# Optimization experiments

Hardware: AMD Instinct MI355X
Metric: run time of the kernel (lower is better)

Reference implementation:

```python
import jax, jax.numpy as jnp
import numpy as np

MIN_NORM = 1e-15
BALL_EPS = 1e-3   # project() margin from ball boundary (c = 1)
TANH_CLIP = 15.0


def _norm(x):
    return jnp.sqrt(jnp.sum(x * x, axis=-1, keepdims=True)).clip(MIN_NORM)


def _tanh(x):
    return jnp.tanh(jnp.clip(x, -TANH_CLIP, TANH_CLIP))


def _artanh(x):
    return jnp.arctanh(jnp.clip(x, -1.0 + 1e-7, 1.0 - 1e-7))


def mobius_add(x, y):
    # Poincare ball Mobius addition, curvature c = 1
    x2 = jnp.sum(x * x, axis=-1, keepdims=True)
    y2 = jnp.sum(y * y, axis=-1, keepdims=True)
    xy = jnp.sum(x * y, axis=-1, keepdims=True)
    num = (1.0 + 2.0 * xy + y2) * x + (1.0 - x2) * y
    den = 1.0 + 2.0 * xy + x2 * y2
    return num / den.clip(MIN_NORM)


def project(x):
    norm = _norm(x)
    maxnorm = 1.0 - BALL_EPS
    return jnp.where(norm > maxnorm, x * (maxnorm / norm), x)


def expmap0(u):
    # exp map at the origin
    n = _norm(u)
    return _tanh(n) * u / n


def expmap(u, p):
    # exp map of tangent vector u at base point p
    n = _norm(u)
    p2 = jnp.sum(p * p, axis=-1, keepdims=True)
    lam = 2.0 / (1.0 - p2).clip(MIN_NORM)
    second = _tanh(0.5 * lam * n) * u / n
    return mobius_add(p, second)


def logmap(y, x):
    # log map of point y at base point x
    sub = mobius_add(-x, y)
    n = _norm(sub)
    x2 = jnp.sum(x * x, axis=-1, keepdims=True)
    lam = 2.0 / (1.0 - x2).clip(MIN_NORM)
    return (2.0 / lam) * _artanh(n) * sub / n


def setup_inputs() -> dict:
    key = jax.random.key(0)
    k1, k2, k3, k4 = jax.random.split(key, 4)
    n_entities, n_edges, n_rel, d = 100000, 800000, 32, 64
    # scale embeddings down so points stay well inside the unit ball
    ego_embed = 0.1 * jax.random.normal(k1, (n_entities, d), dtype=jnp.float32)
    relation_embed = 0.1 * jax.random.normal(k2, (n_rel, d), dtype=jnp.float32)
    edge_index = jax.random.randint(k3, (2, n_edges), 0, n_entities, dtype=jnp.int64)
    edge_type = jax.random.randint(k4, (n_edges,), 0, n_rel, dtype=jnp.int64)
    return {"ego_embed": ego_embed, "edge_index": edge_index,
            "edge_type": edge_type, "relation_embed": relation_embed}


def reference(ego_embed, edge_index, edge_type, relation_embed):
    head, tail = edge_index[0], edge_index[1]
    n_entities = ego_embed.shape[0]
    head_emb = ego_embed[head]          # [E, d] gather
    tail_emb = ego_embed[tail]          # [E, d] gather
    relation_emb = relation_embed[edge_type]  # [E, d] gather
    hyper_head = expmap0(head_emb)
    hyper_tail = expmap(tail_emb, hyper_head)
    hyper_rel = expmap(relation_emb, hyper_head)
    res = project(mobius_add(hyper_tail, hyper_rel))
    res = logmap(res, hyper_head)
    # scatter_mean over head index
    sums = jax.ops.segment_sum(res, head, num_segments=n_entities)
    counts = jax.ops.segment_sum(jnp.ones((head.shape[0],), dtype=res.dtype),
                                 head, num_segments=n_entities)
    entity_agg = sums / jnp.maximum(counts, 1.0)[:, None]
    return entity_agg
```

## Files before the change

kernel.cpp:

```cpp
#include <hip/hip_runtime.h>
#include <math.h>

#define D 64
#define MAXNORM 0.999f
#define MAXNORM2 (0.999f * 0.999f)
#define MIN_NORM 1e-15f
#define TANH_CLIP 15.0f
#define CHUNK 1024

struct f4 { float x, y, z, w; };

__device__ __forceinline__ float frcp(float x) { return __builtin_amdgcn_rcpf(x); }
__device__ __forceinline__ float frsq(float x) { return __builtin_amdgcn_rsqf(x); }

__device__ __forceinline__ float dot8p(const f4& a0, const f4& a1,
                                       const f4& b0, const f4& b1) {
    return a0.x * b0.x + a0.y * b0.y + a0.z * b0.z + a0.w * b0.w +
           a1.x * b1.x + a1.y * b1.y + a1.z * b1.z + a1.w * b1.w;
}

__device__ __forceinline__ float rsum8(float v) {
    v += __shfl_xor(v, 1);
    v += __shfl_xor(v, 2);
    v += __shfl_xor(v, 4);
    return v;
}


__global__ void setup_kernel(const float* __restrict__ ego,
                             const float* __restrict__ rel,
                             const int* __restrict__ eidx,
                             int* __restrict__ cnt,
                             int* __restrict__ rank,
                             float* __restrict__ norms,
                             float* __restrict__ relnorm,
                             int N, int E, int hist_blocks) {
    int b = blockIdx.x;
    if (b < hist_blocks) {
        int e = b * 256 + threadIdx.x;
        if (e < E) rank[e] = atomicAdd(&cnt[eidx[e]], 1);
        return;
    }
    int wid = (b - hist_blocks) * 4 + (threadIdx.x >> 6);
    int lane = threadIdx.x & 63;
    const float* src;
    float* dst;
    if (wid < N)            { src = ego + (size_t)wid * D;       dst = norms + wid; }
    else if (wid < N + 32)  { src = rel + (size_t)(wid - N) * D; dst = relnorm + (wid - N); }
    else return;
    float v = src[lane];
    float s = v * v;
    s += __shfl_xor(s, 1);  s += __shfl_xor(s, 2);  s += __shfl_xor(s, 4);
    s += __shfl_xor(s, 8);  s += __shfl_xor(s, 16); s += __shfl_xor(s, 32);
    if (lane == 0) *dst = sqrtf(s);
}


__global__ void scan_kernel(const int* __restrict__ cnt,
                            int* __restrict__ off, int N) {
    __shared__ int sdata[256];
    __shared__ int sprefix;
    int tid = threadIdx.x;
    int base0 = blockIdx.x * CHUNK;

    int psum = 0;
    const int4* cnt4 = (const int4*)cnt;
    for (int i = tid; i < (base0 >> 2); i += 256) {
        int4 v = cnt4[i];
        psum += v.x + v.y + v.z + v.w;
    }
    sdata[tid] = psum;
    __syncthreads();
    for (int o = 128; o > 0; o >>= 1) {
        if (tid < o) sdata[tid] += sdata[tid + o];
        __syncthreads();
    }
    if (tid == 0) sprefix = sdata[0];
    __syncthreads();
    int prefix = sprefix;
    __syncthreads();

    int base = base0 + tid * 4;
    int v0 = (base + 0 < N) ? cnt[base + 0] : 0;
    int v1 = (base + 1 < N) ? cnt[base + 1] : 0;
    int v2 = (base + 2 < N) ? cnt[base + 2] : 0;
    int v3 = (base + 3 < N) ? cnt[base + 3] : 0;
    sdata[tid] = v0 + v1 + v2 + v3;
    __syncthreads();
    for (int o = 1; o < 256; o <<= 1) {
        int add = (tid >= o) ? sdata[tid - o] : 0;
        __syncthreads();
        sdata[tid] += add;
        __syncthreads();
    }
    int run = prefix + ((tid > 0) ? sdata[tid - 1] : 0);
    if (base + 0 < N) { off[base + 0] = run; run += v0; }
    if (base + 1 < N) { off[base + 1] = run; run += v1; }
    if (base + 2 < N) { off[base + 2] = run; run += v2; }
    if (base + 3 < N) { off[base + 3] = run; run += v3; }
}

__global__ void scatter_kernel(const int* __restrict__ eidx,
                               const int* __restrict__ etype,
                               const int* __restrict__ rank,
                               const int* __restrict__ off,
                               int* __restrict__ sorted, int E) {
    int e = blockIdx.x * blockDim.x + threadIdx.x;
    if (e < E) {
        int pos = off[eidx[e]] + rank[e];
        sorted[pos] = eidx[E + e] | (etype[e] << 17);
    }
}


__global__ void __launch_bounds__(256) agg_kernel(
        const float* __restrict__ ego,
        const float* __restrict__ rel,
        const int* __restrict__ off,
        const int* __restrict__ cnt,
        const int* __restrict__ sorted,
        const float* __restrict__ norms,
        const float* __restrict__ relnorm,
        float* __restrict__ out,
        int N) {
    int wid = (blockIdx.x * blockDim.x + threadIdx.x) >> 6;
    if (wid >= N) return;
    int lane = threadIdx.x & 63;
    int slot = lane >> 3;
    int sub  = lane & 7;

    int h = wid;
    const float* hrow = ego + (size_t)h * D + sub * 8;
    f4 h0 = *(const f4*)(hrow);
    f4 h1 = *(const f4*)(hrow + 4);

    float nh  = fmaxf(norms[h], MIN_NORM);
    float xh  = fminf(nh, TANH_CLIP);
    float eh  = __expf(-2.0f * xh);
    float fp  = (1.0f - eh) * frcp((1.0f + eh) * nh);
    float p2  = fp * fp * nh * nh;
    float tol = fmaxf(1.0f - p2, MIN_NORM);
    float hl  = frcp(tol);

    int o = off[h];
    int c = cnt[h];
    f4 a0 = {0.f, 0.f, 0.f, 0.f}, a1 = {0.f, 0.f, 0.f, 0.f};
    float accP = 0.f;

    for (int i = slot; i < c; i += 8) {
        int pk   = sorted[o + i];
        int tail = pk & 0x1FFFF;
        int type = pk >> 17;

        const float* trow = ego + (size_t)tail * D + sub * 8;
        f4 t0 = *(const f4*)(trow);
        f4 t1 = *(const f4*)(trow + 4);
        const float* rrow = rel + (size_t)type * D + sub * 8;
        f4 r0 = *(const f4*)(rrow);
        f4 r1 = *(const f4*)(rrow + 4);
        float nt = norms[tail];
        float nr = relnorm[type];

        float d_ht = rsum8(dot8p(h0, h1, t0, t1));
        float d_hr = rsum8(dot8p(h0, h1, r0, r1));
        float d_tr = rsum8(dot8p(t0, t1, r0, r1));

        float t2 = nt * nt, r2 = nr * nr;
        float pt = fp * d_ht;
        float pr = fp * d_hr;

        float ntc = fmaxf(nt, MIN_NORM);
        float xt  = fminf(hl * ntc, TANH_CLIP);
        float et  = __expf(-2.0f * xt);
        float ft  = (1.0f - et) * frcp((1.0f + et) * ntc);
        float yt2 = ft * ft * t2;
        float pyt = ft * pt;
        float invt = frcp(fmaxf(1.0f + 2.0f * pyt + p2 * yt2, MIN_NORM));
        float At = (1.0f + 2.0f * pyt + yt2) * invt;
        float Bt = tol * invt * ft;
        float x2 = (p2 + 2.0f * pyt + yt2) * invt;

        float nrc = fmaxf(nr, MIN_NORM);
        float xr  = fminf(hl * nrc, TANH_CLIP);
        float er  = __expf(-2.0f * xr);
        float fr  = (1.0f - er) * frcp((1.0f + er) * nrc);
        float yr2 = fr * fr * r2;
        float pyr = fr * pr;
        float invr = frcp(fmaxf(1.0f + 2.0f * pyr + p2 * yr2, MIN_NORM));
        float Ar = (1.0f + 2.0f * pyr + yr2) * invr;
        float Br = tol * invr * fr;
        float y2 = (p2 + 2.0f * pyr + yr2) * invr;

        float xy = At * Ar * p2 + At * Br * pr + Ar * Bt * pt + Bt * Br * d_tr;
        float am = 1.0f + 2.0f * xy + y2;
        float bm = 1.0f - x2;
        float invm = frcp(fmaxf(1.0f + 2.0f * xy + x2 * y2, MIN_NORM));
        float al = (am * At + bm * Ar) * invm;
        float be = am * Bt * invm;
        float ga = bm * Br * invm;
        float m2 = (x2 + 2.0f * xy + y2) * invm;
        m2 = fmaxf(m2, 1e-30f);

        float scp = (m2 > MAXNORM2) ? MAXNORM * frsq(m2) : 1.0f;
        al *= scp; be *= scp; ga *= scp;
        m2 *= scp * scp;

        float pm   = al * p2 + be * pt + ga * pr;
        float invs = frcp(fmaxf(1.0f - 2.0f * pm + p2 * m2, MIN_NORM));
        float sp   = -(1.0f - 2.0f * pm + m2) * invs;
        float smm  = tol * invs;
        float u = sp + smm * al;
        float v = smm * be;
        float w = smm * ga;
        float s2 = (p2 - 2.0f * pm + m2) * invs;
        s2 = fmaxf(s2, 1e-30f);

        float irs = frsq(s2);
        float ns  = fminf(s2 * irs, 1.0f - 1e-7f);
        float art = 0.5f * __logf((1.0f + ns) * frcp(1.0f - ns));
        float sc  = tol * art * irs;

        float ct = sc * v, cr = sc * w;
        accP += sc * u;
        a0.x += ct * t0.x + cr * r0.x;  a0.y += ct * t0.y + cr * r0.y;
        a0.z += ct * t0.z + cr * r0.z;  a0.w += ct * t0.w + cr * r0.w;
        a1.x += ct * t1.x + cr * r1.x;  a1.y += ct * t1.y + cr * r1.y;
        a1.z += ct * t1.z + cr * r1.z;  a1.w += ct * t1.w + cr * r1.w;
    }

    #define RED(x) x += __shfl_xor(x, 8); x += __shfl_xor(x, 16); x += __shfl_xor(x, 32);
    RED(accP)
    RED(a0.x) RED(a0.y) RED(a0.z) RED(a0.w)
    RED(a1.x) RED(a1.y) RED(a1.z) RED(a1.w)
    #undef RED

    if (slot == 0) {
        float invc = frcp(fmaxf((float)c, 1.0f));
        float hp = accP * fp * invc;
        f4 o0, o1;
        o0.x = hp * h0.x + a0.x * invc;  o0.y = hp * h0.y + a0.y * invc;
        o0.z = hp * h0.z + a0.z * invc;  o0.w = hp * h0.w + a0.w * invc;
        o1.x = hp * h1.x + a1.x * invc;  o1.y = hp * h1.y + a1.y * invc;
        o1.z = hp * h1.z + a1.z * invc;  o1.w = hp * h1.w + a1.w * invc;
        float* orow = out + (size_t)h * D + sub * 8;
        *(f4*)(orow)     = o0;
        *(f4*)(orow + 4) = o1;
    }
}

extern "C" void kernel_launch(void* const* d_in, const int* in_sizes, int n_in,
                              void* d_out, int out_size, void* d_ws, size_t ws_size,
                              hipStream_t stream) {
    const float* ego  = (const float*)d_in[0];
    const int*   eidx = (const int*)d_in[1];
    const int*   etyp = (const int*)d_in[2];
    const float* rel  = (const float*)d_in[3];
    float* out = (float*)d_out;

    int E = in_sizes[1] / 2;
    int N = in_sizes[0] / D;
    int NB = (N + CHUNK - 1) / CHUNK;

    int* cnt      = (int*)d_ws;
    int* off      = cnt + N;
    int* rank     = off + N;
    int* sorted   = rank + E;
    float* norms   = (float*)(sorted + E);
    float* relnorm = norms + N;

    hipMemsetAsync(cnt, 0, (size_t)N * sizeof(int), stream);

    const int tpb = 256;
    int hist_blocks = (E + tpb - 1) / tpb;
    int norm_blocks = (N + 32 + 3) / 4;

    setup_kernel<<<hist_blocks + norm_blocks, tpb, 0, stream>>>(
        ego, rel, eidx, cnt, rank, norms, relnorm, N, E, hist_blocks);
    scan_kernel<<<NB, tpb, 0, stream>>>(cnt, off, N);
    scatter_kernel<<<hist_blocks, tpb, 0, stream>>>(eidx, etyp, rank, off, sorted, E);

    int nblocks = (N + 3) / 4;
    agg_kernel<<<nblocks, tpb, 0, stream>>>(ego, rel, off, cnt, sorted,
                                            norms, relnorm, out, N);
}
```

Baseline: 175.3 us.

## Fuse all stages into one cooperative persistent kernel with grid syncs

Replaces the memset plus four separate kernel launches with a single cooperative kernel that uses grid-wide syncs between the histogram/norm, scan, scatter and aggregation phases. Aggregation becomes a grid-stride loop over heads, and the next packed edge index is prefetched one iteration ahead. This removes launch gaps and the memset, but adds grid.sync barriers and caps the persistent grid at 2048 blocks, which may reduce latency hiding compared with one wave per head.

Result: slower. 448.8 us (+156.0%).

```diff
diff --git a/kernel.cpp b/kernel.cpp
--- a/kernel.cpp
+++ b/kernel.cpp
@@ -1,5 +1,8 @@
 #include <hip/hip_runtime.h>
+#include <hip/hip_cooperative_groups.h>
 #include <math.h>
+
+namespace cg = cooperative_groups;
 
 #define D 64
 #define MAXNORM 0.999f
@@ -26,225 +29,223 @@
     return v;
 }
 
-
-__global__ void setup_kernel(const float* __restrict__ ego,
-                             const float* __restrict__ rel,
-                             const int* __restrict__ eidx,
-                             int* __restrict__ cnt,
-                             int* __restrict__ rank,
-                             float* __restrict__ norms,
-                             float* __restrict__ relnorm,
-                             int N, int E, int hist_blocks) {
-    int b = blockIdx.x;
-    if (b < hist_blocks) {
-        int e = b * 256 + threadIdx.x;
-        if (e < E) rank[e] = atomicAdd(&cnt[eidx[e]], 1);
-        return;
-    }
-    int wid = (b - hist_blocks) * 4 + (threadIdx.x >> 6);
-    int lane = threadIdx.x & 63;
-    const float* src;
-    float* dst;
-    if (wid < N)            { src = ego + (size_t)wid * D;       dst = norms + wid; }
-    else if (wid < N + 32)  { src = rel + (size_t)(wid - N) * D; dst = relnorm + (wid - N); }
-    else return;
-    float v = src[lane];
-    float s = v * v;
-    s += __shfl_xor(s, 1);  s += __shfl_xor(s, 2);  s += __shfl_xor(s, 4);
-    s += __shfl_xor(s, 8);  s += __shfl_xor(s, 16); s += __shfl_xor(s, 32);
-    if (lane == 0) *dst = sqrtf(s);
-}
-
-
-__global__ void scan_kernel(const int* __restrict__ cnt,
-                            int* __restrict__ off, int N) {
+__global__ void __launch_bounds__(256) mega_kernel(
+        const float* __restrict__ ego,
+        const float* __restrict__ rel,
+        const int* __restrict__ eidx,
+        const int* __restrict__ etyp,
+        float* __restrict__ out,
+        int* __restrict__ cnt,
+        int* __restrict__ off,
+        int* __restrict__ rank,
+        int* __restrict__ sorted,
+        float* __restrict__ norms,
+        float* __restrict__ relnorm,
+        int N, int E, int NB) {
+    cg::grid_group grid = cg::this_grid();
     __shared__ int sdata[256];
     __shared__ int sprefix;
-    int tid = threadIdx.x;
-    int base0 = blockIdx.x * CHUNK;
-
-    int psum = 0;
-    const int4* cnt4 = (const int4*)cnt;
-    for (int i = tid; i < (base0 >> 2); i += 256) {
-        int4 v = cnt4[i];
-        psum += v.x + v.y + v.z + v.w;
-    }
-    sdata[tid] = psum;
-    __syncthreads();
-    for (int o = 128; o > 0; o >>= 1) {
-        if (tid < o) sdata[tid] += sdata[tid + o];
-        __syncthreads();
-    }
-    if (tid == 0) sprefix = sdata[0];
-    __syncthreads();
-    int prefix = sprefix;
-    __syncthreads();
-
-    int base = base0 + tid * 4;
-    int v0 = (base + 0 < N) ? cnt[base + 0] : 0;
-    int v1 = (base + 1 < N) ? cnt[base + 1] : 0;
-    int v2 = (base + 2 < N) ? cnt[base + 2] : 0;
-    int v3 = (base + 3 < N) ? cnt[base + 3] : 0;
-    sdata[tid] = v0 + v1 + v2 + v3;
-    __syncthreads();
-    for (int o = 1; o < 256; o <<= 1) {
-        int add = (tid >= o) ? sdata[tid - o] : 0;
-        __syncthreads();
-        sdata[tid] += add;
-        __syncthreads();
-    }
-    int run = prefix + ((tid > 0) ? sdata[tid - 1] : 0);
-    if (base + 0 < N) { off[base + 0] = run; run += v0; }
-    if (base + 1 < N) { off[base + 1] = run; run += v1; }
-    if (base + 2 < N) { off[base + 2] = run; run += v2; }
-    if (base + 3 < N) { off[base + 3] = run; run += v3; }
-}
-
-__global__ void scatter_kernel(const int* __restrict__ eidx,
-                               const int* __restrict__ etype,
-                               const int* __restrict__ rank,
-                               const int* __restrict__ off,
-                               int* __restrict__ sorted, int E) {
-    int e = blockIdx.x * blockDim.x + threadIdx.x;
-    if (e < E) {
+
+    const int tid     = threadIdx.x;
+    const int gthread = blockIdx.x * 256 + tid;
+    const int gsize   = gridDim.x * 256;
+    const int lane    = tid & 63;
+    const int gwave   = gthread >> 6;
+    const int nwave   = gsize >> 6;
+
+    for (int i = gthread; i < N; i += gsize) cnt[i] = 0;
+    grid.sync();
+
+    for (int e = gthread; e < E; e += gsize)
+        rank[e] = atomicAdd(&cnt[eidx[e]], 1);
+    for (int w = gwave; w < N + 32; w += nwave) {
+        const float* src = (w < N) ? (ego + (size_t)w * D)
+                                   : (rel + (size_t)(w - N) * D);
+        float v = src[lane];
+        float s = v * v;
+        s += __shfl_xor(s, 1);  s += __shfl_xor(s, 2);  s += __shfl_xor(s, 4);
+        s += __shfl_xor(s, 8);  s += __shfl_xor(s, 16); s += __shfl_xor(s, 32);
+        if (lane == 0) {
+            if (w < N) norms[w] = sqrtf(s);
+            else       relnorm[w - N] = sqrtf(s);
+        }
+    }
+    grid.sync();
+
+    if (blockIdx.x < NB) {
+        int base0 = blockIdx.x * CHUNK;
+        int psum = 0;
+        const int4* cnt4 = (const int4*)cnt;
+        for (int i = tid; i < (base0 >> 2); i += 256) {
+            int4 v = cnt4[i];
+            psum += v.x + v.y + v.z + v.w;
+        }
+        sdata[tid] = psum;
+        __syncthreads();
+        for (int o = 128; o > 0; o >>= 1) {
+            if (tid < o) sdata[tid] += sdata[tid + o];
+            __syncthreads();
+        }
+        if (tid == 0) sprefix = sdata[0];
+        __syncthreads();
+        int prefix = sprefix;
+        __syncthreads();
+
+        int base = base0 + tid * 4;
+        int v0 = (base + 0 < N) ? cnt[base + 0] : 0;
+        int v1 = (base + 1 < N) ? cnt[base + 1] : 0;
+        int v2 = (base + 2 < N) ? cnt[base + 2] : 0;
+        int v3 = (base + 3 < N) ? cnt[base + 3] : 0;
+        sdata[tid] = v0 + v1 + v2 + v3;
+        __syncthreads();
+        for (int o = 1; o < 256; o <<= 1) {
+            int add = (tid >= o) ? sdata[tid - o] : 0;
+            __syncthreads();
+            sdata[tid] += add;
+            __syncthreads();
+        }
+        int run = prefix + ((tid > 0) ? sdata[tid - 1] : 0);
+        if (base + 0 < N) { off[base + 0] = run; run += v0; }
+        if (base + 1 < N) { off[base + 1] = run; run += v1; }
+        if (base + 2 < N) { off[base + 2] = run; run += v2; }
+        if (base + 3 < N) { off[base + 3] = run; run += v3; }
+    }
+    grid.sync();
+
+    for (int e = gthread; e < E; e += gsize) {
         int pos = off[eidx[e]] + rank[e];
-        sorted[pos] = eidx[E + e] | (etype[e] << 17);
-    }
-}
-
-
-__global__ void __launch_bounds__(256) agg_kernel(
-        const float* __restrict__ ego,
-        const float* __restrict__ rel,
-        const int* __restrict__ off,
-        const int* __restrict__ cnt,
-        const int* __restrict__ sorted,
-        const float* __restrict__ norms,
-        const float* __restrict__ relnorm,
-        float* __restrict__ out,
-        int N) {
-    int wid = (blockIdx.x * blockDim.x + threadIdx.x) >> 6;
-    if (wid >= N) return;
-    int lane = threadIdx.x & 63;
-    int slot = lane >> 3;
-    int sub  = lane & 7;
-
-    int h = wid;
-    const float* hrow = ego + (size_t)h * D + sub * 8;
-    f4 h0 = *(const f4*)(hrow);
-    f4 h1 = *(const f4*)(hrow + 4);
-
-    float nh  = fmaxf(norms[h], MIN_NORM);
-    float xh  = fminf(nh, TANH_CLIP);
-    float eh  = __expf(-2.0f * xh);
-    float fp  = (1.0f - eh) * frcp((1.0f + eh) * nh);
-    float p2  = fp * fp * nh * nh;
-    float tol = fmaxf(1.0f - p2, MIN_NORM);
-    float hl  = frcp(tol);
-
-    int o = off[h];
-    int c = cnt[h];
-    f4 a0 = {0.f, 0.f, 0.f, 0.f}, a1 = {0.f, 0.f, 0.f, 0.f};
-    float accP = 0.f;
-
-    for (int i = slot; i < c; i += 8) {
-        int pk   = sorted[o + i];
-        int tail = pk & 0x1FFFF;
-        int type = pk >> 17;
-
-        const float* trow = ego + (size_t)tail * D + sub * 8;
-        f4 t0 = *(const f4*)(trow);
-        f4 t1 = *(const f4*)(trow + 4);
-        const float* rrow = rel + (size_t)type * D + sub * 8;
-        f4 r0 = *(const f4*)(rrow);
-        f4 r1 = *(const f4*)(rrow + 4);
-        float nt = norms[tail];
-        float nr = relnorm[type];
-
-        float d_ht = rsum8(dot8p(h0, h1, t0, t1));
-        float d_hr = rsum8(dot8p(h0, h1, r0, r1));
-        float d_tr = rsum8(dot8p(t0, t1, r0, r1));
-
-        float t2 = nt * nt, r2 = nr * nr;
-        float pt = fp * d_ht;
-        float pr = fp * d_hr;
-
-        float ntc = fmaxf(nt, MIN_NORM);
-        float xt  = fminf(hl * ntc, TANH_CLIP);
-        float et  = __expf(-2.0f * xt);
-        float ft  = (1.0f - et) * frcp((1.0f + et) * ntc);
-        float yt2 = ft * ft * t2;
-        float pyt = ft * pt;
-        float invt = frcp(fmaxf(1.0f + 2.0f * pyt + p2 * yt2, MIN_NORM));
-        float At = (1.0f + 2.0f * pyt + yt2) * invt;
-        float Bt = tol * invt * ft;
-        float x2 = (p2 + 2.0f * pyt + yt2) * invt;
-
-        float nrc = fmaxf(nr, MIN_NORM);
-        float xr  = fminf(hl * nrc, TANH_CLIP);
-        float er  = __expf(-2.0f * xr);
-        float fr  = (1.0f - er) * frcp((1.0f + er) * nrc);
-        float yr2 = fr * fr * r2;
-        float pyr = fr * pr;
-        float invr = frcp(fmaxf(1.0f + 2.0f * pyr + p2 * yr2, MIN_NORM));
-        float Ar = (1.0f + 2.0f * pyr + yr2) * invr;
-        float Br = tol * invr * fr;
-        float y2 = (p2 + 2.0f * pyr + yr2) * invr;
-
-        float xy = At * Ar * p2 + At * Br * pr + Ar * Bt * pt + Bt * Br * d_tr;
-        float am = 1.0f + 2.0f * xy + y2;
-        float bm = 1.0f - x2;
-        float invm = frcp(fmaxf(1.0f + 2.0f * xy + x2 * y2, MIN_NORM));
-        float al = (am * At + bm * Ar) * invm;
-        float be = am * Bt * invm;
-        float ga = bm * Br * invm;
-        float m2 = (x2 + 2.0f * xy + y2) * invm;
-        m2 = fmaxf(m2, 1e-30f);
-
-        float scp = (m2 > MAXNORM2) ? MAXNORM * frsq(m2) : 1.0f;
-        al *= scp; be *= scp; ga *= scp;
-        m2 *= scp * scp;
-
-        float pm   = al * p2 + be * pt + ga * pr;
-        float invs = frcp(fmaxf(1.0f - 2.0f * pm + p2 * m2, MIN_NORM));
-        float sp   = -(1.0f - 2.0f * pm + m2) * invs;
-        float smm  = tol * invs;
-        float u = sp + smm * al;
-        float v = smm * be;
-        float w = smm * ga;
-        float s2 = (p2 - 2.0f * pm + m2) * invs;
-        s2 = fmaxf(s2, 1e-30f);
-
-        float irs = frsq(s2);
-        float ns  = fminf(s2 * irs, 1.0f - 1e-7f);
-        float art = 0.5f * __logf((1.0f + ns) * frcp(1.0f - ns));
-        float sc  = tol * art * irs;
-
-        float ct = sc * v, cr = sc * w;
-        accP += sc * u;
-        a0.x += ct * t0.x + cr * r0.x;  a0.y += ct * t0.y + cr * r0.y;
-        a0.z += ct * t0.z + cr * r0.z;  a0.w += ct * t0.w + cr * r0.w;
-        a1.x += ct * t1.x + cr * r1.x;  a1.y += ct * t1.y + cr * r1.y;
-        a1.z += ct * t1.z + cr * r1.z;  a1.w += ct * t1.w + cr * r1.w;
-    }
-
-    #define RED(x) x += __shfl_xor(x, 8); x += __shfl_xor(x, 16); x += __shfl_xor(x, 32);
-    RED(accP)
-    RED(a0.x) RED(a0.y) RED(a0.z) RED(a0.w)
-    RED(a1.x) RED(a1.y) RED(a1.z) RED(a1.w)
-    #undef RED
-
-    if (slot == 0) {
-        float invc = frcp(fmaxf((float)c, 1.0f));
-        float hp = accP * fp * invc;
-        f4 o0, o1;
-        o0.x = hp * h0.x + a0.x * invc;  o0.y = hp * h0.y + a0.y * invc;
-        o0.z = hp * h0.z + a0.z * invc;  o0.w = hp * h0.w + a0.w * invc;
-        o1.x = hp * h1.x + a1.x * invc;  o1.y = hp * h1.y + a1.y * invc;
-        o1.z = hp * h1.z + a1.z * invc;  o1.w = hp * h1.w + a1.w * invc;
-        float* orow = out + (size_t)h * D + sub * 8;
-        *(f4*)(orow)     = o0;
-        *(f4*)(orow + 4) = o1;
+        sorted[pos] = eidx[E + e] | (etyp[e] << 17);
+    }
+    grid.sync();
+
+    {
+        const int slot = lane >> 3;
+        const int sub  = lane & 7;
+
+        for (int h = gwave; h < N; h += nwave) {
+            const float* hrow = ego + (size_t)h * D + sub * 8;
+            f4 h0 = *(const f4*)(hrow);
+            f4 h1 = *(const f4*)(hrow + 4);
+
+            float nh  = fmaxf(norms[h], MIN_NORM);
+            float xh  = fminf(nh, TANH_CLIP);
+            float eh  = __expf(-2.0f * xh);
+            float fp  = (1.0f - eh) * frcp((1.0f + eh) * nh);
+            float p2  = fp * fp * nh * nh;
+            float tol = fmaxf(1.0f - p2, MIN_NORM);
+            float hl  = frcp(tol);
+
+            int o = off[h];
+            int c = cnt[h];
+            f4 a0 = {0.f, 0.f, 0.f, 0.f}, a1 = {0.f, 0.f, 0.f, 0.f};
+            float accP = 0.f;
+
+            int i = slot;
+            int pk = (i < c) ? sorted[o + i] : 0;
+            for (; i < c; i += 8) {
+                int inext = i + 8;
+                int pkn = (inext < c) ? sorted[o + inext] : 0;
+
+                int tail = pk & 0x1FFFF;
+                int type = pk >> 17;
+
+                const float* trow = ego + (size_t)tail * D + sub * 8;
+                f4 t0 = *(const f4*)(trow);
+                f4 t1 = *(const f4*)(trow + 4);
+                const float* rrow = rel + (size_t)type * D + sub * 8;
+                f4 r0 = *(const f4*)(rrow);
+                f4 r1 = *(const f4*)(rrow + 4);
+                float nt = norms[tail];
+                float nr = relnorm[type];
+
+                float d_ht = rsum8(dot8p(h0, h1, t0, t1));
+                float d_hr = rsum8(dot8p(h0, h1, r0, r1));
+                float d_tr = rsum8(dot8p(t0, t1, r0, r1));
+
+                float t2 = nt * nt, r2 = nr * nr;
+                float pt = fp * d_ht;
+                float pr = fp * d_hr;
+
+                float ntc = fmaxf(nt, MIN_NORM);
+                float xt  = fminf(hl * ntc, TANH_CLIP);
+                float et  = __expf(-2.0f * xt);
+                float ft  = (1.0f - et) * frcp((1.0f + et) * ntc);
+                float yt2 = ft * ft * t2;
+                float pyt = ft * pt;
+                float invt = frcp(fmaxf(1.0f + 2.0f * pyt + p2 * yt2, MIN_NORM));
+                float At = (1.0f + 2.0f * pyt + yt2) * invt;
+                float Bt = tol * invt * ft;
+                float x2 = (p2 + 2.0f * pyt + yt2) * invt;
+
+                float nrc = fmaxf(nr, MIN_NORM);
+                float xr  = fminf(hl * nrc, TANH_CLIP);
+                float er  = __expf(-2.0f * xr);
+                float fr  = (1.0f - er) * frcp((1.0f + er) * nrc);
+                float yr2 = fr * fr * r2;
+                float pyr = fr * pr;
+                float invr = frcp(fmaxf(1.0f + 2.0f * pyr + p2 * yr2, MIN_NORM));
+                float Ar = (1.0f + 2.0f * pyr + yr2) * invr;
+                float Br = tol * invr * fr;
+                float y2 = (p2 + 2.0f * pyr + yr2) * invr;
+
+                float xy = At * Ar * p2 + At * Br * pr + Ar * Bt * pt + Bt * Br * d_tr;
+                float am = 1.0f + 2.0f * xy + y2;
+                float bm = 1.0f - x2;
+                float invm = frcp(fmaxf(1.0f + 2.0f * xy + x2 * y2, MIN_NORM));
+                float al = (am * At + bm * Ar) * invm;
+                float be = am * Bt * invm;
+                float ga = bm * Br * invm;
+                float m2 = (x2 + 2.0f * xy + y2) * invm;
+                m2 = fmaxf(m2, 1e-30f);
+
+                float scp = (m2 > MAXNORM2) ? MAXNORM * frsq(m2) : 1.0f;
+                al *= scp; be *= scp; ga *= scp;
+                m2 *= scp * scp;
+
+                float pm   = al * p2 + be * pt + ga * pr;
+                float invs = frcp(fmaxf(1.0f - 2.0f * pm + p2 * m2, MIN_NORM));
+                float sp   = -(1.0f - 2.0f * pm + m2) * invs;
+                float smm  = tol * invs;
+                float u = sp + smm * al;
+                float v = smm * be;
+                float w = smm * ga;
+                float s2 = (p2 - 2.0f * pm + m2) * invs;
+                s2 = fmaxf(s2, 1e-30f);
+
+                float irs = frsq(s2);
+                float ns  = fminf(s2 * irs, 1.0f - 1e-7f);
+                float art = 0.5f * __logf((1.0f + ns) * frcp(1.0f - ns));
+                float sc  = tol * art * irs;
+
+                float ct = sc * v, cr = sc * w;
+                accP += sc * u;
+                a0.x += ct * t0.x + cr * r0.x;  a0.y += ct * t0.y + cr * r0.y;
+                a0.z += ct * t0.z + cr * r0.z;  a0.w += ct * t0.w + cr * r0.w;
+                a1.x += ct * t1.x + cr * r1.x;  a1.y += ct * t1.y + cr * r1.y;
+                a1.z += ct * t1.z + cr * r1.z;  a1.w += ct * t1.w + cr * r1.w;
+
+                pk = pkn;
+            }
+
+            #define RED(x) x += __shfl_xor(x, 8); x += __shfl_xor(x, 16); x += __shfl_xor(x, 32);
+            RED(accP)
+            RED(a0.x) RED(a0.y) RED(a0.z) RED(a0.w)
+            RED(a1.x) RED(a1.y) RED(a1.z) RED(a1.w)
+            #undef RED
+
+            if (slot == 0) {
+                float invc = frcp(fmaxf((float)c, 1.0f));
+                float hp = accP * fp * invc;
+                f4 o0, o1;
+                o0.x = hp * h0.x + a0.x * invc;  o0.y = hp * h0.y + a0.y * invc;
+                o0.z = hp * h0.z + a0.z * invc;  o0.w = hp * h0.w + a0.w * invc;
+                o1.x = hp * h1.x + a1.x * invc;  o1.y = hp * h1.y + a1.y * invc;
+                o1.z = hp * h1.z + a1.z * invc;  o1.w = hp * h1.w + a1.w * invc;
+                float* orow = out + (size_t)h * D + sub * 8;
+                *(f4*)(orow)     = o0;
+                *(f4*)(orow + 4) = o1;
+            }
+        }
     }
 }
 
@@ -268,18 +269,17 @@
     float* norms   = (float*)(sorted + E);
     float* relnorm = norms + N;
 
-    hipMemsetAsync(cnt, 0, (size_t)N * sizeof(int), stream);
-
-    const int tpb = 256;
-    int hist_blocks = (E + tpb - 1) / tpb;
-    int norm_blocks = (N + 32 + 3) / 4;
-
-    setup_kernel<<<hist_blocks + norm_blocks, tpb, 0, stream>>>(
-        ego, rel, eidx, cnt, rank, norms, relnorm, N, E, hist_blocks);
-    scan_kernel<<<NB, tpb, 0, stream>>>(cnt, off, N);
-    scatter_kernel<<<hist_blocks, tpb, 0, stream>>>(eidx, etyp, rank, off, sorted, E);
-
-    int nblocks = (N + 3) / 4;
-    agg_kernel<<<nblocks, tpb, 0, stream>>>(ego, rel, off, cnt, sorted,
-                                            norms, relnorm, out, N);
-}
+    int blocksPerCU = 0;
+    hipOccupancyMaxActiveBlocksPerMultiprocessor(&blocksPerCU, mega_kernel, 256, 0);
+    if (blocksPerCU < 1) blocksPerCU = 1;
+    long long g = (long long)blocksPerCU * 256;
+    if (g > 2048) g = 2048;
+    if (g < NB)   g = NB;
+    int grid = (int)g;
+
+    void* args[] = { (void*)&ego, (void*)&rel, (void*)&eidx, (void*)&etyp,
+                     (void*)&out, (void*)&cnt, (void*)&off, (void*)&rank,
+                     (void*)&sorted, (void*)&norms, (void*)&relnorm,
+                     (void*)&N, (void*)&E, (void*)&NB };
+    hipLaunchCooperativeKernel(mega_kernel, dim3(grid), dim3(256), args, 0, stream);
+}
```

## Prefetch next edge rows in agg loop and move norm pass into scan launch

Applied to the files above, without the earlier changes.

The aggregation loop now software-pipelines its gathers. It loads the next edge's tail row, relation row and norms while computing the current edge, to hide gather latency. The per-row norm computation moves out of the histogram launch and runs as extra blocks of the scan launch. This keeps the small scan grid busy with independent work and leaves the atomic histogram on its own. The agg kernel also gains a min-blocks launch bound of 4, which limits registers, while the prefetch buffers raise register pressure and could cause spills.

After: 171.6 us. 2.1% less time.

```diff
diff --git a/kernel.cpp b/kernel.cpp
--- a/kernel.cpp
+++ b/kernel.cpp
@@ -27,37 +27,37 @@
 }
 
 
-__global__ void setup_kernel(const float* __restrict__ ego,
-                             const float* __restrict__ rel,
-                             const int* __restrict__ eidx,
-                             int* __restrict__ cnt,
-                             int* __restrict__ rank,
-                             float* __restrict__ norms,
-                             float* __restrict__ relnorm,
-                             int N, int E, int hist_blocks) {
-    int b = blockIdx.x;
-    if (b < hist_blocks) {
-        int e = b * 256 + threadIdx.x;
-        if (e < E) rank[e] = atomicAdd(&cnt[eidx[e]], 1);
+__global__ void hist_kernel(const int* __restrict__ eidx,
+                            int* __restrict__ cnt,
+                            int* __restrict__ rank, int E) {
+    int e = blockIdx.x * blockDim.x + threadIdx.x;
+    if (e < E) rank[e] = atomicAdd(&cnt[eidx[e]], 1);
+}
+
+
+__global__ void scan_kernel(const int* __restrict__ cnt,
+                            int* __restrict__ off,
+                            const float* __restrict__ ego,
+                            const float* __restrict__ rel,
+                            float* __restrict__ norms,
+                            float* __restrict__ relnorm,
+                            int N, int NB) {
+    if (blockIdx.x >= NB) {
+        int wid = (blockIdx.x - NB) * 4 + (threadIdx.x >> 6);
+        int lane = threadIdx.x & 63;
+        const float* src;
+        float* dst;
+        if (wid < N)            { src = ego + (size_t)wid * D;       dst = norms + wid; }
+        else if (wid < N + 32)  { src = rel + (size_t)(wid - N) * D; dst = relnorm + (wid - N); }
+        else return;
+        float v = src[lane];
+        float s = v * v;
+        s += __shfl_xor(s, 1);  s += __shfl_xor(s, 2);  s += __shfl_xor(s, 4);
+        s += __shfl_xor(s, 8);  s += __shfl_xor(s, 16); s += __shfl_xor(s, 32);
+        if (lane == 0) *dst = sqrtf(s);
         return;
     }
-    int wid = (b - hist_blocks) * 4 + (threadIdx.x >> 6);
-    int lane = threadIdx.x & 63;
-    const float* src;
-    float* dst;
-    if (wid < N)            { src = ego + (size_t)wid * D;       dst = norms + wid; }
-    else if (wid < N + 32)  { src = rel + (size_t)(wid - N) * D; dst = relnorm + (wid - N); }
-    else return;
-    float v = src[lane];
-    float s = v * v;
-    s += __shfl_xor(s, 1);  s += __shfl_xor(s, 2);  s += __shfl_xor(s, 4);
-    s += __shfl_xor(s, 8);  s += __shfl_xor(s, 16); s += __shfl_xor(s, 32);
-    if (lane == 0) *dst = sqrtf(s);
-}
-
-
-__global__ void scan_kernel(const int* __restrict__ cnt,
-                            int* __restrict__ off, int N) {
+
     __shared__ int sdata[256];
     __shared__ int sprefix;
     int tid = threadIdx.x;
@@ -113,7 +113,7 @@
 }
 
 
-__global__ void __launch_bounds__(256) agg_kernel(
+__global__ void __launch_bounds__(256, 4) agg_kernel(
         const float* __restrict__ ego,
         const float* __restrict__ rel,
         const int* __restrict__ off,
@@ -147,19 +147,42 @@
     f4 a0 = {0.f, 0.f, 0.f, 0.f}, a1 = {0.f, 0.f, 0.f, 0.f};
     float accP = 0.f;
 
-    for (int i = slot; i < c; i += 8) {
+    int i = slot;
+    bool act = (i < c);
+    f4 t0, t1, r0, r1;
+    float nt = 1.0f, nr = 1.0f;
+    if (act) {
         int pk   = sorted[o + i];
         int tail = pk & 0x1FFFF;
         int type = pk >> 17;
-
         const float* trow = ego + (size_t)tail * D + sub * 8;
-        f4 t0 = *(const f4*)(trow);
-        f4 t1 = *(const f4*)(trow + 4);
+        t0 = *(const f4*)(trow);
+        t1 = *(const f4*)(trow + 4);
         const float* rrow = rel + (size_t)type * D + sub * 8;
-        f4 r0 = *(const f4*)(rrow);
-        f4 r1 = *(const f4*)(rrow + 4);
-        float nt = norms[tail];
-        float nr = relnorm[type];
+        r0 = *(const f4*)(rrow);
+        r1 = *(const f4*)(rrow + 4);
+        nt = norms[tail];
+        nr = relnorm[type];
+    }
+
+    while (act) {
+        int inext = i + 8;
+        bool actn = (inext < c);
+        f4 pt0, pt1, pr0, pr1;
+        float ntn = 1.0f, nrn = 1.0f;
+        if (actn) {
+            int pkn   = sorted[o + inext];
+            int tailn = pkn & 0x1FFFF;
+            int typen = pkn >> 17;
+            const float* trown = ego + (size_t)tailn * D + sub * 8;
+            pt0 = *(const f4*)(trown);
+            pt1 = *(const f4*)(trown + 4);
+            const float* rrown = rel + (size_t)typen * D + sub * 8;
+            pr0 = *(const f4*)(rrown);
+            pr1 = *(const f4*)(rrown + 4);
+            ntn = norms[tailn];
+            nrn = relnorm[typen];
+        }
 
         float d_ht = rsum8(dot8p(h0, h1, t0, t1));
         float d_hr = rsum8(dot8p(h0, h1, r0, r1));
@@ -226,6 +249,9 @@
         a0.z += ct * t0.z + cr * r0.z;  a0.w += ct * t0.w + cr * r0.w;
         a1.x += ct * t1.x + cr * r1.x;  a1.y += ct * t1.y + cr * r1.y;
         a1.z += ct * t1.z + cr * r1.z;  a1.w += ct * t1.w + cr * r1.w;
+
+        i = inext; act = actn;
+        t0 = pt0; t1 = pt1; r0 = pr0; r1 = pr1; nt = ntn; nr = nrn;
     }
 
     #define RED(x) x += __shfl_xor(x, 8); x += __shfl_xor(x, 16); x += __shfl_xor(x, 32);
@@ -274,9 +300,9 @@
     int hist_blocks = (E + tpb - 1) / tpb;
     int norm_blocks = (N + 32 + 3) / 4;
 
-    setup_kernel<<<hist_blocks + norm_blocks, tpb, 0, stream>>>(
-        ego, rel, eidx, cnt, rank, norms, relnorm, N, E, hist_blocks);
-    scan_kernel<<<NB, tpb, 0, stream>>>(cnt, off, N);
+    hist_kernel<<<hist_blocks, tpb, 0, stream>>>(eidx, cnt, rank, E);
+    scan_kernel<<<NB + norm_blocks, tpb, 0, stream>>>(cnt, off, ego, rel,
+                                                      norms, relnorm, N, NB);
     scatter_kernel<<<hist_blocks, tpb, 0, stream>>>(eidx, etyp, rank, off, sorted, E);
 
     int nblocks = (N + 3) / 4;
```

## Move norm pass into scan kernel, precompute head scalars, simplify edge math

Applied to the files above, without the earlier changes.

Splits the histogram out of the setup kernel and folds the entity/relation norm computation into the scan kernel launch. The scan kernel now also precomputes per-head expmap0 scalars (fp, tol), which the aggregation kernel reads instead of recomputing. Edge counts now come from adjacent offsets, with off[N]=E, rather than a separate cnt load. The per-edge math is rewritten algebraically with FMAs and shared subexpressions to cut instruction count, at the cost of slightly different rounding.

Result: faster. 167.0 us (-4.8%).

```diff
diff --git a/kernel.cpp b/kernel.cpp
--- a/kernel.cpp
+++ b/kernel.cpp
@@ -27,41 +27,55 @@
 }
 
 
-__global__ void setup_kernel(const float* __restrict__ ego,
-                             const float* __restrict__ rel,
-                             const int* __restrict__ eidx,
-                             int* __restrict__ cnt,
-                             int* __restrict__ rank,
-                             float* __restrict__ norms,
-                             float* __restrict__ relnorm,
-                             int N, int E, int hist_blocks) {
-    int b = blockIdx.x;
-    if (b < hist_blocks) {
-        int e = b * 256 + threadIdx.x;
-        if (e < E) rank[e] = atomicAdd(&cnt[eidx[e]], 1);
+__global__ void hist_kernel(const int* __restrict__ eidx,
+                            int* __restrict__ cnt,
+                            int* __restrict__ rank, int E) {
+    int e = blockIdx.x * blockDim.x + threadIdx.x;
+    if (e < E) rank[e] = atomicAdd(&cnt[eidx[e]], 1);
+}
+
+
+__global__ void scan_kernel(const int* __restrict__ cnt,
+                            int* __restrict__ off,
+                            const float* __restrict__ ego,
+                            const float* __restrict__ rel,
+                            float* __restrict__ norms,
+                            float* __restrict__ relnorm,
+                            float2* __restrict__ scal,
+                            int N, int NB, int E) {
+    if (blockIdx.x >= NB) {
+        int wid = (blockIdx.x - NB) * 4 + (threadIdx.x >> 6);
+        int lane = threadIdx.x & 63;
+        if (wid >= N + 32) return;
+        const float* src = (wid < N) ? (ego + (size_t)wid * D)
+                                     : (rel + (size_t)(wid - N) * D);
+        float v = src[lane];
+        float s = v * v;
+        s += __shfl_xor(s, 1);  s += __shfl_xor(s, 2);  s += __shfl_xor(s, 4);
+        s += __shfl_xor(s, 8);  s += __shfl_xor(s, 16); s += __shfl_xor(s, 32);
+        if (lane == 0) {
+            float nh = sqrtf(s);
+            if (wid < N) {
+                norms[wid] = nh;
+                float nhc = fmaxf(nh, MIN_NORM);
+                float eh  = __expf(-2.0f * fminf(nhc, TANH_CLIP));
+                float fp  = (1.0f - eh) * frcp((1.0f + eh) * nhc);
+                float th2 = fp * fp * nhc * nhc;
+                float tol = fmaxf(1.0f - th2, MIN_NORM);
+                scal[wid] = make_float2(fp, tol);
+            } else {
+                relnorm[wid - N] = nh;
+            }
+        }
         return;
     }
-    int wid = (b - hist_blocks) * 4 + (threadIdx.x >> 6);
-    int lane = threadIdx.x & 63;
-    const float* src;
-    float* dst;
-    if (wid < N)            { src = ego + (size_t)wid * D;       dst = norms + wid; }
-    else if (wid < N + 32)  { src = rel + (size_t)(wid - N) * D; dst = relnorm + (wid - N); }
-    else return;
-    float v = src[lane];
-    float s = v * v;
-    s += __shfl_xor(s, 1);  s += __shfl_xor(s, 2);  s += __shfl_xor(s, 4);
-    s += __shfl_xor(s, 8);  s += __shfl_xor(s, 16); s += __shfl_xor(s, 32);
-    if (lane == 0) *dst = sqrtf(s);
-}
-
-
-__global__ void scan_kernel(const int* __restrict__ cnt,
-                            int* __restrict__ off, int N) {
+
     __shared__ int sdata[256];
     __shared__ int sprefix;
     int tid = threadIdx.x;
     int base0 = blockIdx.x * CHUNK;
+
+    if (blockIdx.x == 0 && tid == 0) off[N] = E;
 
     int psum = 0;
     const int4* cnt4 = (const int4*)cnt;
@@ -117,10 +131,10 @@
         const float* __restrict__ ego,
         const float* __restrict__ rel,
         const int* __restrict__ off,
-        const int* __restrict__ cnt,
         const int* __restrict__ sorted,
         const float* __restrict__ norms,
         const float* __restrict__ relnorm,
+        const float2* __restrict__ scal,
         float* __restrict__ out,
         int N) {
     int wid = (blockIdx.x * blockDim.x + threadIdx.x) >> 6;
@@ -134,16 +148,14 @@
     f4 h0 = *(const f4*)(hrow);
     f4 h1 = *(const f4*)(hrow + 4);
 
-    float nh  = fmaxf(norms[h], MIN_NORM);
-    float xh  = fminf(nh, TANH_CLIP);
-    float eh  = __expf(-2.0f * xh);
-    float fp  = (1.0f - eh) * frcp((1.0f + eh) * nh);
-    float p2  = fp * fp * nh * nh;
-    float tol = fmaxf(1.0f - p2, MIN_NORM);
+    float2 sc2 = scal[h];
+    float fp  = sc2.x;
+    float tol = sc2.y;
+    float p2  = 1.0f - tol;
     float hl  = frcp(tol);
 
     int o = off[h];
-    int c = cnt[h];
+    int c = off[h + 1] - o;
     f4 a0 = {0.f, 0.f, 0.f, 0.f}, a1 = {0.f, 0.f, 0.f, 0.f};
     float accP = 0.f;
 
@@ -170,58 +182,62 @@
         float pr = fp * d_hr;
 
         float ntc = fmaxf(nt, MIN_NORM);
-        float xt  = fminf(hl * ntc, TANH_CLIP);
-        float et  = __expf(-2.0f * xt);
+        float et  = __expf(-2.0f * fminf(hl * ntc, TANH_CLIP));
         float ft  = (1.0f - et) * frcp((1.0f + et) * ntc);
+        float pyt = ft * pt;
         float yt2 = ft * ft * t2;
-        float pyt = ft * pt;
-        float invt = frcp(fmaxf(1.0f + 2.0f * pyt + p2 * yt2, MIN_NORM));
-        float At = (1.0f + 2.0f * pyt + yt2) * invt;
+        float o1t = fmaf(2.0f, pyt, 1.0f);
+        float at  = o1t + yt2;
+        float invt = frcp(fmaxf(fmaf(p2, yt2, o1t), MIN_NORM));
+        float At = at * invt;
         float Bt = tol * invt * ft;
-        float x2 = (p2 + 2.0f * pyt + yt2) * invt;
+        float x2 = (at - tol) * invt;
 
         float nrc = fmaxf(nr, MIN_NORM);
-        float xr  = fminf(hl * nrc, TANH_CLIP);
-        float er  = __expf(-2.0f * xr);
+        float er  = __expf(-2.0f * fminf(hl * nrc, TANH_CLIP));
         float fr  = (1.0f - er) * frcp((1.0f + er) * nrc);
+        float pyr = fr * pr;
         float yr2 = fr * fr * r2;
-        float pyr = fr * pr;
-        float invr = frcp(fmaxf(1.0f + 2.0f * pyr + p2 * yr2, MIN_NORM));
-        float Ar = (1.0f + 2.0f * pyr + yr2) * invr;
+        float o1r = fmaf(2.0f, pyr, 1.0f);
+        float ar  = o1r + yr2;
+        float invr = frcp(fmaxf(fmaf(p2, yr2, o1r), MIN_NORM));
+        float Ar = ar * invr;
         float Br = tol * invr * fr;
-        float y2 = (p2 + 2.0f * pyr + yr2) * invr;
+        float y2 = (ar - tol) * invr;
 
         float xy = At * Ar * p2 + At * Br * pr + Ar * Bt * pt + Bt * Br * d_tr;
-        float am = 1.0f + 2.0f * xy + y2;
+        float o1m = fmaf(2.0f, xy, 1.0f);
+        float am = o1m + y2;
         float bm = 1.0f - x2;
-        float invm = frcp(fmaxf(1.0f + 2.0f * xy + x2 * y2, MIN_NORM));
+        float invm = frcp(fmaxf(fmaf(x2, y2, o1m), MIN_NORM));
         float al = (am * At + bm * Ar) * invm;
         float be = am * Bt * invm;
         float ga = bm * Br * invm;
-        float m2 = (x2 + 2.0f * xy + y2) * invm;
-        m2 = fmaxf(m2, 1e-30f);
-
-        float scp = (m2 > MAXNORM2) ? MAXNORM * frsq(m2) : 1.0f;
-        al *= scp; be *= scp; ga *= scp;
-        m2 *= scp * scp;
+        float m2 = fmaxf((am - bm) * invm, 1e-30f);
+
+        if (m2 > MAXNORM2) {
+            float s_ = MAXNORM * frsq(m2);
+            al *= s_; be *= s_; ga *= s_;
+            m2 = MAXNORM2;
+        }
 
         float pm   = al * p2 + be * pt + ga * pr;
-        float invs = frcp(fmaxf(1.0f - 2.0f * pm + p2 * m2, MIN_NORM));
-        float sp   = -(1.0f - 2.0f * pm + m2) * invs;
+        float o2   = fmaf(-2.0f, pm, 1.0f);
+        float invs = frcp(fmaxf(fmaf(p2, m2, o2), MIN_NORM));
+        float om   = o2 + m2;
         float smm  = tol * invs;
-        float u = sp + smm * al;
+        float u = fmaf(smm, al, -om * invs);
         float v = smm * be;
         float w = smm * ga;
-        float s2 = (p2 - 2.0f * pm + m2) * invs;
-        s2 = fmaxf(s2, 1e-30f);
+        float s2 = fmaxf((om - tol) * invs, 1e-30f);
 
         float irs = frsq(s2);
         float ns  = fminf(s2 * irs, 1.0f - 1e-7f);
         float art = 0.5f * __logf((1.0f + ns) * frcp(1.0f - ns));
-        float sc  = tol * art * irs;
-
-        float ct = sc * v, cr = sc * w;
-        accP += sc * u;
+        float scv = tol * art * irs;
+
+        float ct = scv * v, cr = scv * w;
+        accP = fmaf(scv, u, accP);
         a0.x += ct * t0.x + cr * r0.x;  a0.y += ct * t0.y + cr * r0.y;
         a0.z += ct * t0.z + cr * r0.z;  a0.w += ct * t0.w + cr * r0.w;
         a1.x += ct * t1.x + cr * r1.x;  a1.y += ct * t1.y + cr * r1.y;
@@ -261,9 +277,10 @@
     int N = in_sizes[0] / D;
     int NB = (N + CHUNK - 1) / CHUNK;
 
-    int* cnt      = (int*)d_ws;
+    float2* scal  = (float2*)d_ws;
+    int* cnt      = (int*)(scal + N);
     int* off      = cnt + N;
-    int* rank     = off + N;
+    int* rank     = off + N + 1;
     int* sorted   = rank + E;
     float* norms   = (float*)(sorted + E);
     float* relnorm = norms + N;
@@ -274,12 +291,13 @@
     int hist_blocks = (E + tpb - 1) / tpb;
     int norm_blocks = (N + 32 + 3) / 4;
 
-    setup_kernel<<<hist_blocks + norm_blocks, tpb, 0, stream>>>(
-        ego, rel, eidx, cnt, rank, norms, relnorm, N, E, hist_blocks);
-    scan_kernel<<<NB, tpb, 0, stream>>>(cnt, off, N);
+    hist_kernel<<<hist_blocks, tpb, 0, stream>>>(eidx, cnt, rank, E);
+    scan_kernel<<<NB + norm_blocks, tpb, 0, stream>>>(cnt, off, ego, rel,
+                                                      norms, relnorm, scal,
+                                                      N, NB, E);
     scatter_kernel<<<hist_blocks, tpb, 0, stream>>>(eidx, etyp, rank, off, sorted, E);
 
     int nblocks = (N + 3) / 4;
-    agg_kernel<<<nblocks, tpb, 0, stream>>>(ego, rel, off, cnt, sorted,
-                                            norms, relnorm, out, N);
-}
+    agg_kernel<<<nblocks, tpb, 0, stream>>>(ego, rel, off, sorted,
+                                            norms, relnorm, scal, out, N);
+}
```
